# Performance work log

Measured on AMD Instinct MI355X. Metric: run time of the kernel, lower is better.

## Reference

```python
import jax, jax.numpy as jnp
import numpy as np

NUM_HEADS = 12
QUAD_C = 5.0

def setup_inputs() -> dict:
    key = jax.random.key(0)
    k1, k2, k3 = jax.random.split(key, 3)
    B, N, C = 8, 1024, 768
    x = jax.random.normal(k1, (B, N, C), dtype=jnp.float32)
    qkv_w = jax.random.normal(k2, (3 * C, C), dtype=jnp.float32) * (C ** -0.5)
    proj_w = jax.random.normal(k3, (C, C), dtype=jnp.float32) * (C ** -0.5)
    proj_b = jnp.zeros((C,), dtype=jnp.float32)
    return {"x": x, "qkv_w": qkv_w, "proj_w": proj_w, "proj_b": proj_b}

def reference(x, qkv_w, proj_w, proj_b):
    B, N, C = x.shape
    H = NUM_HEADS
    hd = C // H
    scale = hd ** -0.5
    # qkv projection: [B,N,3C] -> [3,B,H,N,hd]
    qkv = (x @ qkv_w.T).reshape(B, N, 3, H, hd).transpose(2, 0, 3, 1, 4)
    q, k, v = qkv[0], qkv[1], qkv[2]
    # explicit N x N attention scores
    attn = jnp.einsum('bhnd,bhmd->bhnm', q, k) * scale
    # Quad2 normalization: square(x + c) / row-sum
    t = jnp.square(attn + QUAD_C)
    attn = t / jnp.sum(t, axis=-1, keepdims=True)
    out = jnp.einsum('bhnm,bhmd->bhnd', attn, v)  # [B,H,N,hd]
    out = out.transpose(0, 2, 1, 3).reshape(B, N, C)
    return out @ proj_w.T + proj_b
```

## Files before the change

### kernel.cpp

```cpp
#include <hip/hip_runtime.h>
#include <hip/hip_bf16.h>
#include <stdint.h>


typedef short  s8v  __attribute__((ext_vector_type(8)));
typedef float  f4v  __attribute__((ext_vector_type(4)));

__device__ inline uint16_t f2bf(float f) {
    union { float f; uint32_t u; } c; c.f = f;
    uint32_t u = c.u;
    u += 0x7fffu + ((u >> 16) & 1u);
    return (uint16_t)(u >> 16);
}
__device__ inline uint32_t pack2bf(float a, float b) {
    union { __hip_bfloat162 v; uint32_t u; } c;
    c.v = __float22bfloat162_rn(float2{a, b});
    return c.u;
}

__device__ inline void cp16(const uint16_t* g, uint16_t* l) {
    __builtin_amdgcn_global_load_lds(
        (const __attribute__((address_space(1))) void*)g,
        (__attribute__((address_space(3))) void*)l, 16, 0, 0);
}

__global__ __launch_bounds__(256) void cvt_all(
    const float* __restrict__ x, const float* __restrict__ qw,
    const float* __restrict__ pw, uint16_t* __restrict__ dst)
{
    int i = blockIdx.x * 256 + threadIdx.x;
    if (i >= 1081344) return;
    const float* s;
    if (i < 786432)       s = x  + (size_t)i * 8;
    else if (i < 1007616) s = qw + ((size_t)i - 786432) * 8;
    else                  s = pw + ((size_t)i - 1007616) * 8;
    const float4* sp = reinterpret_cast<const float4*>(s);
    float4 a = sp[0], b = sp[1];
    s8v o;
    o[0] = (short)f2bf(a.x); o[1] = (short)f2bf(a.y);
    o[2] = (short)f2bf(a.z); o[3] = (short)f2bf(a.w);
    o[4] = (short)f2bf(b.x); o[5] = (short)f2bf(b.y);
    o[6] = (short)f2bf(b.z); o[7] = (short)f2bf(b.w);
    *reinterpret_cast<s8v*>(dst + (size_t)i * 8) = o;
}

template <int EPI>
__global__ __launch_bounds__(256) void gemm_m97(
    const uint16_t* __restrict__ A, const uint16_t* __restrict__ Bm,
    uint16_t* __restrict__ qb, uint16_t* __restrict__ kb, uint16_t* __restrict__ vb,
    const float* __restrict__ bias, float* __restrict__ Cout, int GN)
{
    constexpr int K  = 768;
    constexpr int NT = K / 64;

    __shared__ uint16_t Al[128 * 64];
    __shared__ uint16_t Bl[128 * 64];

    const int tid  = threadIdx.x;
    const int wave = tid >> 6, lane = tid & 63;
    const int quad = lane >> 4, l16 = lane & 15;
    const int wM = wave >> 1, wN = wave & 1;

    const int nwg = (int)gridDim.x;
    const int wg  = ((int)blockIdx.x & 7) * (nwg >> 3) + ((int)blockIdx.x >> 3);
    const int bM = wg / GN, bN = wg - bM * GN;

    const uint16_t* Ag = A  + (size_t)bM * 128 * K;
    const uint16_t* Bg = Bm + (size_t)bN * 128 * K;

    f4v acc[4][4];
#pragma unroll
    for (int i = 0; i < 4; i++)
#pragma unroll
        for (int j = 0; j < 4; j++) { f4v z = {0.f, 0.f, 0.f, 0.f}; acc[i][j] = z; }

    for (int t = 0; t < NT; ++t) {
        __syncthreads();
#pragma unroll
        for (int u = 0; u < 4; ++u) {
            const int ch = tid + u * 256;
            const int r  = ch >> 3, lc = (ch & 7) ^ (r & 7);
            cp16(Ag + (size_t)r * K + t * 64 + lc * 8, &Al[ch * 8]);
        }
#pragma unroll
        for (int u = 0; u < 4; ++u) {
            const int ch = tid + u * 256;
            const int r  = ch >> 3, lc = (ch & 7) ^ (r & 7);
            cp16(Bg + (size_t)r * K + t * 64 + lc * 8, &Bl[ch * 8]);
        }
        __syncthreads();

        s8v af[4][2], bq[4][2];
#pragma unroll
        for (int x = 0; x < 4; ++x) {
            const int ra = wM * 64 + x * 16 + l16;
            const int rb = wN * 64 + x * 16 + l16;
#pragma unroll
            for (int kk = 0; kk < 2; ++kk) {
                const int pa = (kk * 4 + quad) ^ (ra & 7);
                const int pb = (kk * 4 + quad) ^ (rb & 7);
                af[x][kk] = *reinterpret_cast<const s8v*>(&Al[ra * 64 + pa * 8]);
                bq[x][kk] = *reinterpret_cast<const s8v*>(&Bl[rb * 64 + pb * 8]);
            }
        }
#pragma unroll
        for (int kk = 0; kk < 2; ++kk)
#pragma unroll
            for (int tm = 0; tm < 4; ++tm)
#pragma unroll
                for (int tn = 0; tn < 4; ++tn)
                    acc[tm][tn] = __builtin_amdgcn_mfma_f32_16x16x32_bf16(
                        af[tm][kk], bq[tn][kk], acc[tm][tn], 0, 0, 0);
    }

#pragma unroll
    for (int tm = 0; tm < 4; tm++) {
#pragma unroll
        for (int tn = 0; tn < 4; tn++) {
            const int col = bN * 128 + wN * 64 + tn * 16 + l16;
            if (EPI == 0) {
                const int three = col / 768;
                const int rem   = col - three * 768;
                const int h = rem >> 6, d = rem & 63;
                const int n0 = bM * 128 + wM * 64 + tm * 16 + quad * 4;
                const int b = n0 >> 10, n = n0 & 1023;
                if (three == 2) {
                    ushort4 pk;
                    pk.x = f2bf(acc[tm][tn][0]);
                    pk.y = f2bf(acc[tm][tn][1]);
                    pk.z = f2bf(acc[tm][tn][2]);
                    pk.w = f2bf(acc[tm][tn][3]);
                    *reinterpret_cast<ushort4*>(
                        &vb[((size_t)((b * 12 + h) * 64 + d)) * 1024 + n]) = pk;
                } else {
                    uint16_t* dst = (three == 0) ? qb : kb;
#pragma unroll
                    for (int reg = 0; reg < 4; reg++)
                        dst[((size_t)((b * 12 + h) * 1024 + n + reg)) * 64 + d] =
                            f2bf(acc[tm][tn][reg]);
                }
            } else {
#pragma unroll
                for (int reg = 0; reg < 4; reg++) {
                    const int row = bM * 128 + wM * 64 + tm * 16 + quad * 4 + reg;
                    Cout[(size_t)row * 768 + col] = acc[tm][tn][reg] + bias[col];
                }
            }
        }
    }
}

__global__ __launch_bounds__(128, 2) void attn_quad(
    const uint16_t* __restrict__ Q, const uint16_t* __restrict__ K,
    const uint16_t* __restrict__ VT, uint16_t* __restrict__ O)
{
    const int qt = blockIdx.x;
    const int bh = blockIdx.y;
    const int b = bh / 12, h = bh - (bh / 12) * 12;
    const uint16_t* Qp = Q  + (size_t)bh * 65536;
    const uint16_t* Kp = K  + (size_t)bh * 65536;
    const uint16_t* Vp = VT + (size_t)bh * 65536;

    const int tid  = threadIdx.x;
    const int wave = tid >> 6, lane = tid & 63;
    const int quad = lane >> 4, l16 = lane & 15;

    __shared__ uint16_t Kl[64 * 64];
    __shared__ uint16_t Vl[64 * 64];
    __shared__ uint16_t Pl[2][16][80];

    s8v qf[4][2];
#pragma unroll
    for (int s = 0; s < 4; s++) {
        const uint16_t* qp = Qp + (size_t)(qt * 128 + wave * 64 + s * 16 + l16) * 64 + quad * 8;
        qf[s][0] = *reinterpret_cast<const s8v*>(qp);
        qf[s][1] = *reinterpret_cast<const s8v*>(qp + 32);
    }

    s8v ones;
#pragma unroll
    for (int i = 0; i < 8; i++) ones[i] = (short)0x3F80;

    f4v U[4][4], U5[4];
#pragma unroll
    for (int s = 0; s < 4; s++) {
        f4v z = {0.f, 0.f, 0.f, 0.f};
        U5[s] = z;
#pragma unroll
        for (int c = 0; c < 4; c++) U[s][c] = z;
    }

    for (int mt = 0; mt < 16; mt++) {
        __syncthreads();
#pragma unroll
        for (int r = 0; r < 4; r++) {
            const int e   = (tid + r * 128) * 8;
            const int row = e >> 6;
            const int cl  = ((e >> 3) & 7) ^ (row & 7);
            cp16(Kp + (size_t)mt * 4096 + (size_t)row * 64 + cl * 8, &Kl[e]);
            cp16(Vp + (size_t)row * 1024 + mt * 64 + cl * 8, &Vl[e]);
        }
        __syncthreads();

        s8v kf[4][2], vf[4][2];
#pragma unroll
        for (int c = 0; c < 4; c++) {
            const int rr = c * 16 + l16;
#pragma unroll
            for (int kk = 0; kk < 2; kk++) {
                const int pc = (kk * 4 + quad) ^ (rr & 7);
                kf[c][kk] = *reinterpret_cast<const s8v*>(&Kl[rr * 64 + (pc << 3)]);
                vf[c][kk] = *reinterpret_cast<const s8v*>(&Vl[rr * 64 + (pc << 3)]);
            }
        }

#pragma unroll
        for (int s = 0; s < 4; s++) {
            f4v st[4];
#pragma unroll
            for (int cm = 0; cm < 4; cm++) {
                f4v z = {0.f, 0.f, 0.f, 0.f};
                z = __builtin_amdgcn_mfma_f32_16x16x32_bf16(kf[cm][0], qf[s][0], z, 0, 0, 0);
                z = __builtin_amdgcn_mfma_f32_16x16x32_bf16(kf[cm][1], qf[s][1], z, 0, 0, 0);
                st[cm] = z;
            }
#pragma unroll
            for (int cm = 0; cm < 4; cm++) {
                float t0 = st[cm][0] * 0.125f + 5.0f; t0 *= t0;
                float t1 = st[cm][1] * 0.125f + 5.0f; t1 *= t1;
                float t2 = st[cm][2] * 0.125f + 5.0f; t2 *= t2;
                float t3 = st[cm][3] * 0.125f + 5.0f; t3 *= t3;
                uint2 pk; pk.x = pack2bf(t0, t1); pk.y = pack2bf(t2, t3);
                *reinterpret_cast<uint2*>(&Pl[wave][l16][cm * 16 + quad * 4]) = pk;
            }
#pragma unroll
            for (int kc = 0; kc < 2; kc++) {
                s8v pf = *reinterpret_cast<const s8v*>(&Pl[wave][l16][kc * 32 + quad * 8]);
                U5[s] = __builtin_amdgcn_mfma_f32_16x16x32_bf16(pf, ones, U5[s], 0, 0, 0);
#pragma unroll
                for (int cd = 0; cd < 4; cd++)
                    U[s][cd] = __builtin_amdgcn_mfma_f32_16x16x32_bf16(pf, vf[cd][kc], U[s][cd], 0, 0, 0);
            }
        }
    }

#pragma unroll
    for (int s = 0; s < 4; s++) {
        float inv[4];
#pragma unroll
        for (int reg = 0; reg < 4; reg++) inv[reg] = 1.0f / U5[s][reg];
#pragma unroll
        for (int cd = 0; cd < 4; cd++) {
#pragma unroll
            for (int reg = 0; reg < 4; reg++) {
                const int n = qt * 128 + wave * 64 + s * 16 + quad * 4 + reg;
                const int d = cd * 16 + l16;
                O[((size_t)(b * 1024 + n)) * 768 + h * 64 + d] = f2bf(U[s][cd][reg] * inv[reg]);
            }
        }
    }
}

extern "C" void kernel_launch(void* const* d_in, const int* in_sizes, int n_in,
                              void* d_out, int out_size, void* d_ws, size_t ws_size,
                              hipStream_t stream)
{
    const float* x      = (const float*)d_in[0];
    const float* qkv_w  = (const float*)d_in[1];
    const float* proj_w = (const float*)d_in[2];
    const float* proj_b = (const float*)d_in[3];
    float* out = (float*)d_out;

    const size_t NEL = (size_t)8 * 1024 * 768;
    uint16_t* xb  = (uint16_t*)d_ws;
    uint16_t* qwb = xb  + NEL;
    uint16_t* pwb = qwb + 1769472;
    uint16_t* qb  = pwb + 589824;
    uint16_t* kb  = qb  + NEL;
    uint16_t* vb  = kb  + NEL;
    uint16_t* ao  = vb  + NEL;

    cvt_all<<<4224, 256, 0, stream>>>(x, qkv_w, proj_w, xb);

    gemm_m97<0><<<1152, 256, 0, stream>>>(xb, qwb, qb, kb, vb, nullptr, nullptr, 18);
    attn_quad<<<dim3(8, 96), 128, 0, stream>>>(qb, kb, vb, ao);
    gemm_m97<1><<<384, 256, 0, stream>>>(ao, pwb, nullptr, nullptr, nullptr, proj_b, out, 6);
}
```

Measured before the change: 185.9 us.

## Split GEMM kernels, double-buffer attention K/V and use 4 waves per block

The QKV projection now uses a simpler GEMM with 32-wide K tiles, no swizzle and no block remapping, while the output projection keeps the old 64-wide-tile kernel as a separate function. The attention kernel moves from 2 to 4 waves per 128-query block, with each wave handling 32 query rows. It also double-buffers the K/V tiles in LDS so the next tile's async loads overlap compute on the current one. This aims to hide global-load latency and raise occupancy in attention. In exchange it uses more LDS, K/V fragment reads are repeated across more waves, and the simpler QKV GEMM may lose efficiency.

New measurement: 192.5 us. 3.6% more time.

```diff
diff --git a/kernel.cpp b/kernel.cpp
--- a/kernel.cpp
+++ b/kernel.cpp
@@ -44,10 +44,84 @@
     *reinterpret_cast<s8v*>(dst + (size_t)i * 8) = o;
 }
 
-template <int EPI>
-__global__ __launch_bounds__(256) void gemm_m97(
+__global__ __launch_bounds__(256) void gemm_bt(
     const uint16_t* __restrict__ A, const uint16_t* __restrict__ Bm,
     uint16_t* __restrict__ qb, uint16_t* __restrict__ kb, uint16_t* __restrict__ vb,
+    int K)
+{
+    __shared__ uint16_t Al[128 * 32];
+    __shared__ uint16_t Bl[128 * 32];
+
+    const int tid  = threadIdx.x;
+    const int wave = tid >> 6, lane = tid & 63;
+    const int quad = lane >> 4, l16 = lane & 15;
+    const int wM = wave >> 1, wN = wave & 1;
+    const int bM = blockIdx.x, bN = blockIdx.y;
+
+    f4v acc[4][4];
+#pragma unroll
+    for (int i = 0; i < 4; i++)
+#pragma unroll
+        for (int j = 0; j < 4; j++) { f4v z = {0.f, 0.f, 0.f, 0.f}; acc[i][j] = z; }
+
+    const uint16_t* Ag = A  + (size_t)bM * 128 * K;
+    const uint16_t* Bg = Bm + (size_t)bN * 128 * K;
+
+    const int e0 = tid * 8;
+    const int r0 = e0 >> 5, c0 = e0 & 31;
+
+    for (int kc = 0; kc < K; kc += 32) {
+        __syncthreads();
+        cp16(Ag + (size_t)r0 * K + kc + c0,        &Al[e0]);
+        cp16(Ag + (size_t)(r0 + 64) * K + kc + c0, &Al[e0 + 2048]);
+        cp16(Bg + (size_t)r0 * K + kc + c0,        &Bl[e0]);
+        cp16(Bg + (size_t)(r0 + 64) * K + kc + c0, &Bl[e0 + 2048]);
+        __syncthreads();
+
+        s8v af[4], bf[4];
+#pragma unroll
+        for (int t = 0; t < 4; t++) {
+            af[t] = *reinterpret_cast<const s8v*>(&Al[(wM * 64 + t * 16 + l16) * 32 + quad * 8]);
+            bf[t] = *reinterpret_cast<const s8v*>(&Bl[(wN * 64 + t * 16 + l16) * 32 + quad * 8]);
+        }
+#pragma unroll
+        for (int tm = 0; tm < 4; tm++)
+#pragma unroll
+            for (int tn = 0; tn < 4; tn++)
+                acc[tm][tn] = __builtin_amdgcn_mfma_f32_16x16x32_bf16(af[tm], bf[tn], acc[tm][tn], 0, 0, 0);
+    }
+
+#pragma unroll
+    for (int tm = 0; tm < 4; tm++) {
+#pragma unroll
+        for (int tn = 0; tn < 4; tn++) {
+            const int col = bN * 128 + wN * 64 + tn * 16 + l16;
+            const int three = col / 768;
+            const int rem   = col - three * 768;
+            const int h = rem >> 6, d = rem & 63;
+            const int n0 = bM * 128 + wM * 64 + tm * 16 + quad * 4;
+            const int b = n0 >> 10, n = n0 & 1023;
+            if (three == 2) {
+                ushort4 pk;
+                pk.x = f2bf(acc[tm][tn][0]);
+                pk.y = f2bf(acc[tm][tn][1]);
+                pk.z = f2bf(acc[tm][tn][2]);
+                pk.w = f2bf(acc[tm][tn][3]);
+                *reinterpret_cast<ushort4*>(
+                    &vb[((size_t)((b * 12 + h) * 64 + d)) * 1024 + n]) = pk;
+            } else {
+                uint16_t* dst = (three == 0) ? qb : kb;
+#pragma unroll
+                for (int reg = 0; reg < 4; reg++)
+                    dst[((size_t)((b * 12 + h) * 1024 + n + reg)) * 64 + d] =
+                        f2bf(acc[tm][tn][reg]);
+            }
+        }
+    }
+}
+
+__global__ __launch_bounds__(256) void gemm_proj(
+    const uint16_t* __restrict__ A, const uint16_t* __restrict__ Bm,
     const float* __restrict__ bias, float* __restrict__ Cout, int GN)
 {
     constexpr int K  = 768;
@@ -118,39 +192,16 @@
 #pragma unroll
         for (int tn = 0; tn < 4; tn++) {
             const int col = bN * 128 + wN * 64 + tn * 16 + l16;
-            if (EPI == 0) {
-                const int three = col / 768;
-                const int rem   = col - three * 768;
-                const int h = rem >> 6, d = rem & 63;
-                const int n0 = bM * 128 + wM * 64 + tm * 16 + quad * 4;
-                const int b = n0 >> 10, n = n0 & 1023;
-                if (three == 2) {
-                    ushort4 pk;
-                    pk.x = f2bf(acc[tm][tn][0]);
-                    pk.y = f2bf(acc[tm][tn][1]);
-                    pk.z = f2bf(acc[tm][tn][2]);
-                    pk.w = f2bf(acc[tm][tn][3]);
-                    *reinterpret_cast<ushort4*>(
-                        &vb[((size_t)((b * 12 + h) * 64 + d)) * 1024 + n]) = pk;
-                } else {
-                    uint16_t* dst = (three == 0) ? qb : kb;
-#pragma unroll
-                    for (int reg = 0; reg < 4; reg++)
-                        dst[((size_t)((b * 12 + h) * 1024 + n + reg)) * 64 + d] =
-                            f2bf(acc[tm][tn][reg]);
-                }
-            } else {
-#pragma unroll
-                for (int reg = 0; reg < 4; reg++) {
-                    const int row = bM * 128 + wM * 64 + tm * 16 + quad * 4 + reg;
-                    Cout[(size_t)row * 768 + col] = acc[tm][tn][reg] + bias[col];
-                }
-            }
-        }
-    }
-}
-
-__global__ __launch_bounds__(128, 2) void attn_quad(
+#pragma unroll
+            for (int reg = 0; reg < 4; reg++) {
+                const int row = bM * 128 + wM * 64 + tm * 16 + quad * 4 + reg;
+                Cout[(size_t)row * 768 + col] = acc[tm][tn][reg] + bias[col];
+            }
+        }
+    }
+}
+
+__global__ __launch_bounds__(256, 2) void attn_quad(
     const uint16_t* __restrict__ Q, const uint16_t* __restrict__ K,
     const uint16_t* __restrict__ VT, uint16_t* __restrict__ O)
 {
@@ -165,14 +216,14 @@
     const int wave = tid >> 6, lane = tid & 63;
     const int quad = lane >> 4, l16 = lane & 15;
 
-    __shared__ uint16_t Kl[64 * 64];
-    __shared__ uint16_t Vl[64 * 64];
-    __shared__ uint16_t Pl[2][16][80];
-
-    s8v qf[4][2];
-#pragma unroll
-    for (int s = 0; s < 4; s++) {
-        const uint16_t* qp = Qp + (size_t)(qt * 128 + wave * 64 + s * 16 + l16) * 64 + quad * 8;
+    __shared__ uint16_t Kl[2][64 * 64];
+    __shared__ uint16_t Vl[2][64 * 64];
+    __shared__ uint16_t Pl[4][16][80];
+
+    s8v qf[2][2];
+#pragma unroll
+    for (int s = 0; s < 2; s++) {
+        const uint16_t* qp = Qp + (size_t)(qt * 128 + wave * 32 + s * 16 + l16) * 64 + quad * 8;
         qf[s][0] = *reinterpret_cast<const s8v*>(qp);
         qf[s][1] = *reinterpret_cast<const s8v*>(qp + 32);
     }
@@ -181,26 +232,32 @@
 #pragma unroll
     for (int i = 0; i < 8; i++) ones[i] = (short)0x3F80;
 
-    f4v U[4][4], U5[4];
-#pragma unroll
-    for (int s = 0; s < 4; s++) {
+    f4v U[2][4], U5[2];
+#pragma unroll
+    for (int s = 0; s < 2; s++) {
         f4v z = {0.f, 0.f, 0.f, 0.f};
         U5[s] = z;
 #pragma unroll
         for (int c = 0; c < 4; c++) U[s][c] = z;
     }
 
-    for (int mt = 0; mt < 16; mt++) {
-        __syncthreads();
-#pragma unroll
-        for (int r = 0; r < 4; r++) {
-            const int e   = (tid + r * 128) * 8;
+    auto stage = [&](int mt, int slot) {
+#pragma unroll
+        for (int r = 0; r < 2; ++r) {
+            const int e   = (tid + r * 256) * 8;
             const int row = e >> 6;
             const int cl  = ((e >> 3) & 7) ^ (row & 7);
-            cp16(Kp + (size_t)mt * 4096 + (size_t)row * 64 + cl * 8, &Kl[e]);
-            cp16(Vp + (size_t)row * 1024 + mt * 64 + cl * 8, &Vl[e]);
-        }
-        __syncthreads();
+            cp16(Kp + (size_t)mt * 4096 + (size_t)row * 64 + cl * 8, &Kl[slot][e]);
+            cp16(Vp + (size_t)row * 1024 + mt * 64 + cl * 8, &Vl[slot][e]);
+        }
+    };
+
+    stage(0, 0);
+    __syncthreads();
+
+    int cur = 0;
+    for (int mt = 0; mt < 16; mt++) {
+        if (mt + 1 < 16) stage(mt + 1, cur ^ 1);
 
         s8v kf[4][2], vf[4][2];
 #pragma unroll
@@ -209,13 +266,13 @@
 #pragma unroll
             for (int kk = 0; kk < 2; kk++) {
                 const int pc = (kk * 4 + quad) ^ (rr & 7);
-                kf[c][kk] = *reinterpret_cast<const s8v*>(&Kl[rr * 64 + (pc << 3)]);
-                vf[c][kk] = *reinterpret_cast<const s8v*>(&Vl[rr * 64 + (pc << 3)]);
-            }
-        }
-
-#pragma unroll
-        for (int s = 0; s < 4; s++) {
+                kf[c][kk] = *reinterpret_cast<const s8v*>(&Kl[cur][rr * 64 + (pc << 3)]);
+                vf[c][kk] = *reinterpret_cast<const s8v*>(&Vl[cur][rr * 64 + (pc << 3)]);
+            }
+        }
+
+#pragma unroll
+        for (int s = 0; s < 2; s++) {
             f4v st[4];
 #pragma unroll
             for (int cm = 0; cm < 4; cm++) {
@@ -242,10 +299,13 @@
                     U[s][cd] = __builtin_amdgcn_mfma_f32_16x16x32_bf16(pf, vf[cd][kc], U[s][cd], 0, 0, 0);
             }
         }
-    }
-
-#pragma unroll
-    for (int s = 0; s < 4; s++) {
+
+        __syncthreads();
+        cur ^= 1;
+    }
+
+#pragma unroll
+    for (int s = 0; s < 2; s++) {
         float inv[4];
 #pragma unroll
         for (int reg = 0; reg < 4; reg++) inv[reg] = 1.0f / U5[s][reg];
@@ -253,7 +313,7 @@
         for (int cd = 0; cd < 4; cd++) {
 #pragma unroll
             for (int reg = 0; reg < 4; reg++) {
-                const int n = qt * 128 + wave * 64 + s * 16 + quad * 4 + reg;
+                const int n = qt * 128 + wave * 32 + s * 16 + quad * 4 + reg;
                 const int d = cd * 16 + l16;
                 O[((size_t)(b * 1024 + n)) * 768 + h * 64 + d] = f2bf(U[s][cd][reg] * inv[reg]);
             }
@@ -282,7 +342,7 @@
 
     cvt_all<<<4224, 256, 0, stream>>>(x, qkv_w, proj_w, xb);
 
-    gemm_m97<0><<<1152, 256, 0, stream>>>(xb, qwb, qb, kb, vb, nullptr, nullptr, 18);
-    attn_quad<<<dim3(8, 96), 128, 0, stream>>>(qb, kb, vb, ao);
-    gemm_m97<1><<<384, 256, 0, stream>>>(ao, pwb, nullptr, nullptr, nullptr, proj_b, out, 6);
-}
+    gemm_bt<<<dim3(64, 18), 256, 0, stream>>>(xb, qwb, qb, kb, vb, 768);
+    attn_quad<<<dim3(8, 96), 256, 0, stream>>>(qb, kb, vb, ao);
+    gemm_proj<<<384, 256, 0, stream>>>(ao, pwb, proj_b, out, 6);
+}
```
